# Optimization experiments

Hardware: AMD Instinct MI355X
Metric: run time of the kernel (lower is better)

Reference implementation:

```python
import jax, jax.numpy as jnp
from jax import lax
import numpy as np

EPS = 1e-5  # BatchNorm eps


def setup_inputs() -> dict:
    key = jax.random.key(0)
    ks = jax.random.split(key, 8)
    N, C_in, T, V = 64, 64, 300, 25
    C_out, K, KT = 64, 3, 9
    x = jax.random.normal(ks[0], (N, C_in, T, V), dtype=jnp.float32)
    A = jax.random.uniform(ks[1], (K, V, V), dtype=jnp.float32)
    # 1x1 conv weight squeezed to [K*C_out, C_in]
    w_gcn = jax.random.normal(ks[2], (K * C_out, C_in), dtype=jnp.float32) * (1.0 / np.sqrt(C_in))
    b_gcn = jax.random.normal(ks[3], (K * C_out,), dtype=jnp.float32) * 0.01
    # temporal conv weight [O, I, kT, 1]
    w_tcn = jax.random.normal(ks[4], (C_out, C_out, KT, 1), dtype=jnp.float32) * (1.0 / np.sqrt(C_out * KT))
    b_tcn = jax.random.normal(ks[5], (C_out,), dtype=jnp.float32) * 0.01
    gamma = jnp.ones((C_out,), dtype=jnp.float32)
    beta = jnp.zeros((C_out,), dtype=jnp.float32)
    return {"x": x, "A": A, "w_gcn": w_gcn, "b_gcn": b_gcn,
            "w_tcn": w_tcn, "b_tcn": b_tcn, "gamma": gamma, "beta": beta}


def reference(x, A, w_gcn, b_gcn, w_tcn, b_tcn, gamma, beta):
    K = A.shape[0]
    # unit_gcn: 1x1 conv (pointwise over channels) then spatial graph aggregation
    y = jnp.einsum('nctv,oc->notv', x, w_gcn) + b_gcn[None, :, None, None]  # [N, K*C, T, V]
    n, kc, t, v = y.shape
    y = y.reshape(n, K, kc // K, t, v)
    y = jnp.einsum('nkctv,kvw->nctw', y, A)  # [N, C, T, V]
    # unit_tcn: temporal conv (kernel 9x1, pad 4) + BatchNorm (training mode: batch stats)
    pad = (w_tcn.shape[2] - 1) // 2
    y = lax.conv_general_dilated(y, w_tcn, window_strides=(1, 1),
                                 padding=((pad, pad), (0, 0)),
                                 dimension_numbers=('NCHW', 'OIHW', 'NCHW'))
    y = y + b_tcn[None, :, None, None]
    mean = jnp.mean(y, axis=(0, 2, 3), keepdims=True)
    var = jnp.var(y, axis=(0, 2, 3), keepdims=True)
    y = (y - mean) * lax.rsqrt(var + EPS) * gamma[None, :, None, None] + beta[None, :, None, None]
    # residual (identity: in==out, stride==1) + ReLU
    return jax.nn.relu(y + x)
```

## Files before the change

### kernel.cpp

```cpp
#include <hip/hip_runtime.h>
#include <hip/hip_bf16.h>

#define N_    64
#define C_    64
#define T_    300
#define V_    25
#define K_    3
#define KT_   9
#define PAD_  4

typedef short bf16x8 __attribute__((ext_vector_type(8)));
typedef float f32x4  __attribute__((ext_vector_type(4)));

static __device__ __forceinline__ unsigned short f2bf(float f) {
    __hip_bfloat16 h = __float2bfloat16(f);
    return __builtin_bit_cast(unsigned short, h);
}
static __device__ __forceinline__ unsigned int pk2(float a, float b) {
    return (unsigned int)f2bf(a) | ((unsigned int)f2bf(b) << 16);
}
static __device__ __forceinline__ float bfhi(unsigned int u) {
    return __builtin_bit_cast(float, u << 16);
}
static __device__ __forceinline__ float bflo(unsigned int u) {
    return __builtin_bit_cast(float, u & 0xffff0000u);
}
static __device__ __forceinline__ float bf2f(unsigned short u) {
    return __builtin_bit_cast(float, (unsigned int)u << 16);
}

__global__ __launch_bounds__(256) void prep_kernel(
    const float* __restrict__ Wt, const float* __restrict__ Wg,
    const float* __restrict__ bg, const float* __restrict__ A,
    unsigned short* __restrict__ Wtb, unsigned short* __restrict__ Wgbt,
    unsigned short* __restrict__ bias2b, unsigned short* __restrict__ Abt)
{
    int i = blockIdx.x * 256 + threadIdx.x;
    if (i < 9*64*64) {
        int kt = i >> 12, r = i & 4095, o = r >> 6, c = r & 63;
        Wtb[i] = f2bf(Wt[(size_t)(o*64 + c)*9 + kt]);
    }
    int j = i - 9*64*64;
    if (j >= 0 && j < 64*192) {
        int o = j / 192, kc = j - 192*(j/192);
        int k = kc >> 6, ci = kc & 63;
        Wgbt[j] = f2bf(Wg[(size_t)(k*64 + o)*64 + ci]);
    }
    int m = j - 64*192;
    if (m >= 0 && m < 64*25) {
        int c = m / 25, w = m - 25*(m/25);
        float s = 0.f;
        for (int k = 0; k < 3; ++k) {
            float col = 0.f;
            for (int v = 0; v < 25; ++v) col += A[k*625 + v*25 + w];
            s += bg[k*64 + c] * col;
        }
        bias2b[w*64 + c] = f2bf(s);
    }
    int p = m - 64*25;
    if (p >= 0 && p < 3*32*40) {
        int k = p / 1280, r = p - 1280*k, w = r / 40, v = r - 40*(r/40);
        float val = (w < 25 && v < 25) ? A[k*625 + v*25 + w] : 0.f;
        Abt[p] = f2bf(val);
    }
}

#define GSUB   15
#define GGRP   (T_/GSUB)
#define NGBLK  (N_*GGRP)

__global__ __launch_bounds__(256, 5) void gcn_kernel(
    const float* __restrict__ x,
    const unsigned short* __restrict__ Wgbt,
    const unsigned short* __restrict__ Abt,
    const unsigned short* __restrict__ bias2b,
    unsigned short* __restrict__ y2)
{
    __shared__ unsigned short xslab[64*40];
    __shared__ unsigned short xa[32*200];
    __shared__ unsigned int   bias2L[25*34];

    const int tid  = threadIdx.x;
    const int n    = blockIdx.x / GGRP;
    const int tg   = (blockIdx.x % GGRP) * GSUB;
    const int lane = tid & 63, wave = tid >> 6;
    const int l15  = lane & 15, lq = lane >> 4;

    bf16x8 wfrag[6], afrag[6];
    #pragma unroll
    for (int cb = 0; cb < 6; ++cb) {
        wfrag[cb] = *(const bf16x8*)(Wgbt + (wave*16 + l15)*192 + cb*32 + lq*8);
        asm volatile("" : "+v"(wfrag[cb]));
    }
    #pragma unroll
    for (int s = 0; s < 6; ++s) {
        afrag[s] = *(const bf16x8*)(Abt + ((s >> 1)*32 + (s & 1)*16 + l15)*40 + lq*8);
        asm volatile("" : "+v"(afrag[s]));
    }

    for (int i = tid; i < 800; i += 256)
        bias2L[(i >> 5)*34 + (i & 31)] = ((const unsigned int*)bias2b)[i];
    if (tid < 192) {
        int r = tid / 3, z = tid - 3*(tid/3);
        ((unsigned int*)xslab)[r*20 + 13 + z] = 0u;
    }
    #pragma unroll
    for (int s = 0; s < 4; ++s) {
        int slot = tid + s*256;
        if (slot < 64*13) {
            int row = slot/13, sl = slot - 13*row;
            const float* xr = x + ((size_t)(n*C_ + row)*T_ + tg)*V_;
            float f0, f1;
            if (sl < 12) { float2 t2 = *(const float2*)(xr + 2*sl); f0 = t2.x; f1 = t2.y; }
            else         { f0 = xr[24]; f1 = 0.f; }
            ((unsigned int*)xslab)[row*20 + sl] = pk2(f0, f1);
        }
    }
    __syncthreads();

    for (int j = 0; j < GSUB; ++j) {
        const int t = tg + j;
        float2 Lr[4];
        const bool hn = (j + 1 < GSUB);
        if (hn) {
            #pragma unroll
            for (int s = 0; s < 4; ++s) {
                int slot = tid + s*256;
                if (slot < 64*13) {
                    int row = slot/13, sl = slot - 13*row;
                    const float* xr = x + ((size_t)(n*C_ + row)*T_ + t + 1)*V_;
                    if (sl < 12) Lr[s] = *(const float2*)(xr + 2*sl);
                    else         { Lr[s].x = xr[24]; Lr[s].y = 0.f; }
                }
            }
        }
        {
            bf16x8 xf = *(const bf16x8*)(xslab + (wave*16 + l15)*40 + lq*8);
            #pragma unroll
            for (int s = 0; s < 6; ++s) {
                f32x4 d = {};
                d = __builtin_amdgcn_mfma_f32_16x16x32_bf16(xf, afrag[s], d, 0, 0, 0);
                const int w = (s & 1)*16 + l15;
                if (w < 25) {
                    const int k = s >> 1;
                    unsigned long long pv = (unsigned long long)pk2(d[0], d[1])
                                          | ((unsigned long long)pk2(d[2], d[3]) << 32);
                    *(unsigned long long*)((char*)xa + w*400 + k*128 + wave*32 + lq*8) = pv;
                }
            }
        }
        __syncthreads();
        {
            f32x4 acc0 = {}, acc1 = {};
            #pragma unroll
            for (int cb = 0; cb < 6; ++cb) {
                bf16x8 b0 = *(const bf16x8*)((const char*)xa + l15*400      + cb*64 + lq*16);
                bf16x8 b1 = *(const bf16x8*)((const char*)xa + (16+l15)*400 + cb*64 + lq*16);
                acc0 = __builtin_amdgcn_mfma_f32_16x16x32_bf16(wfrag[cb], b0, acc0, 0, 0, 0);
                acc1 = __builtin_amdgcn_mfma_f32_16x16x32_bf16(wfrag[cb], b1, acc1, 0, 0, 0);
            }
            const int o0 = wave*16 + lq*4;
            {
                const int col = l15;
                unsigned int bu0 = bias2L[col*34 + (o0 >> 1)];
                unsigned int bu1 = bias2L[col*34 + (o0 >> 1) + 1];
                float v0 = acc0[0] + bfhi(bu0), v1 = acc0[1] + bflo(bu0);
                float v2 = acc0[2] + bfhi(bu1), v3 = acc0[3] + bflo(bu1);
                const size_t gcol = ((size_t)n*T_ + t)*V_ + col;
                *(unsigned long long*)(y2 + gcol*64 + o0) =
                      (unsigned long long)pk2(v0, v1)
                    | ((unsigned long long)pk2(v2, v3) << 32);
            }
            if (l15 < 9) {
                const int col = 16 + l15;
                unsigned int bu0 = bias2L[col*34 + (o0 >> 1)];
                unsigned int bu1 = bias2L[col*34 + (o0 >> 1) + 1];
                float v0 = acc1[0] + bfhi(bu0), v1 = acc1[1] + bflo(bu0);
                float v2 = acc1[2] + bfhi(bu1), v3 = acc1[3] + bflo(bu1);
                const size_t gcol = ((size_t)n*T_ + t)*V_ + col;
                *(unsigned long long*)(y2 + gcol*64 + o0) =
                      (unsigned long long)pk2(v0, v1)
                    | ((unsigned long long)pk2(v2, v3) << 32);
            }
        }
        if (hn) {
            #pragma unroll
            for (int s = 0; s < 4; ++s) {
                int slot = tid + s*256;
                if (slot < 64*13) {
                    int row = slot/13, sl = slot - 13*row;
                    ((unsigned int*)xslab)[row*20 + sl] = pk2(Lr[s].x, Lr[s].y);
                }
            }
        }
        __syncthreads();
    }
}

#define TTT    20
#define TCOLS  (TTT*V_)
#define SLABC  712
#define TTILES (T_/TTT)
#define NBLK   (N_*TTILES)

template<int BF>
__global__ __launch_bounds__(512, 2) void tcn_kernel(
    const unsigned short* __restrict__ y2, const unsigned short* __restrict__ Wtb,
    const float* __restrict__ bt,
    unsigned short* __restrict__ y3b, float* __restrict__ y3f,
    float* __restrict__ psum, float* __restrict__ psq)
{
    __shared__ unsigned short slab[SLABC*40];
    __shared__ float s_sum[64], s_sq[64];

    const int tid = threadIdx.x;
    const int n  = blockIdx.x / TTILES;
    const int t0 = (blockIdx.x % TTILES) * TTT;
    const int lane = tid & 63, wave = tid >> 6;
    const int l15 = lane & 15, lq = lane >> 4;
    const int colw = wave * 64;

    if (tid < 64) { s_sum[tid] = 0.f; s_sq[tid] = 0.f; }

    const int lo = (t0 < PAD_) ? (PAD_ - t0)*V_ : 0;
    const int hi = (t0 + TTT + PAD_ > T_) ? (T_ + PAD_ - t0)*V_ : SLABC;
    const long gbase = ((long)n*T_*V_ + (long)(t0 - PAD_)*V_)*64;

    f32x4 acc[4][4] = {};

    #pragma unroll
    for (int h = 0; h < 2; ++h) {
        __syncthreads();
        for (int i = tid; i < SLABC*4; i += 512) {
            int col = i >> 2, ck = i & 3;
            float4 val = {0.f, 0.f, 0.f, 0.f};
            if (col >= lo && col < hi)
                val = *(const float4*)(y2 + gbase + (long)col*64 + h*32 + ck*8);
            *(float4*)((char*)slab + col*80 + ck*16) = val;
        }
        __syncthreads();
        #pragma unroll
        for (int kt = 0; kt < 9; ++kt) {
            bf16x8 a[4];
            #pragma unroll
            for (int mt = 0; mt < 4; ++mt)
                a[mt] = *(const bf16x8*)(Wtb + kt*4096 + (mt*16 + l15)*64
                                         + h*32 + lq*8);
            #pragma unroll
            for (int nf = 0; nf < 4; ++nf) {
                const int col = colw + nf*16 + l15 + kt*25;
                bf16x8 b = *(const bf16x8*)((const char*)slab + col*80 + lq*16);
                #pragma unroll
                for (int mt = 0; mt < 4; ++mt)
                    acc[mt][nf] = __builtin_amdgcn_mfma_f32_16x16x32_bf16(
                        a[mt], b, acc[mt][nf], 0, 0, 0);
            }
        }
    }

    float ls[16], lsq[16];
    #pragma unroll
    for (int e = 0; e < 16; ++e) { ls[e] = 0.f; lsq[e] = 0.f; }

    #pragma unroll
    for (int mt = 0; mt < 4; ++mt) {
        #pragma unroll
        for (int r = 0; r < 4; ++r) {
            const int e = mt*4 + r;
            const int o = mt*16 + lq*4 + r;
            const float bias = bt[o];
            #pragma unroll
            for (int nf = 0; nf < 4; ++nf) {
                const int col = colw + nf*16 + l15;
                if (col < TCOLS) {
                    const float val = acc[mt][nf][r] + bias;
                    const size_t idx = (size_t)(n*C_ + o)*(T_*V_) + t0*V_ + col;
                    if (BF) y3b[idx] = f2bf(val);
                    else    y3f[idx] = val;
                    ls[e] += val; lsq[e] += val*val;
                }
            }
        }
    }

    __syncthreads();
    #pragma unroll
    for (int e = 0; e < 16; ++e) {
        float a = ls[e], b = lsq[e];
        a += __shfl_xor(a, 1); a += __shfl_xor(a, 2);
        a += __shfl_xor(a, 4); a += __shfl_xor(a, 8);
        b += __shfl_xor(b, 1); b += __shfl_xor(b, 2);
        b += __shfl_xor(b, 4); b += __shfl_xor(b, 8);
        if (l15 == 0) {
            const int o = (e >> 2)*16 + lq*4 + (e & 3);
            atomicAdd(&s_sum[o], a);
            atomicAdd(&s_sq[o], b);
        }
    }
    __syncthreads();
    if (tid < 64) {
        psum[(size_t)tid*NBLK + blockIdx.x] = s_sum[tid];
        psq [(size_t)tid*NBLK + blockIdx.x] = s_sq [tid];
    }
}

__global__ __launch_bounds__(256) void stats_kernel(
    const float* __restrict__ psum, const float* __restrict__ psq,
    const float* __restrict__ gamma, const float* __restrict__ beta,
    float* __restrict__ sb)
{
    const int o = blockIdx.x;
    const int tid = threadIdx.x;
    float s = 0.f, q = 0.f;
    for (int i = tid; i < NBLK; i += 256) {
        s += psum[(size_t)o*NBLK + i];
        q += psq [(size_t)o*NBLK + i];
    }
    __shared__ float rs[256], rq[256];
    rs[tid] = s; rq[tid] = q;
    __syncthreads();
    for (int off = 128; off > 0; off >>= 1) {
        if (tid < off) { rs[tid] += rs[tid + off]; rq[tid] += rq[tid + off]; }
        __syncthreads();
    }
    if (tid == 0) {
        const float cnt = (float)(N_ * T_ * V_);
        float mean = rs[0] / cnt;
        float var  = rq[0] / cnt - mean * mean;
        float rstd = rsqrtf(var + 1e-5f);
        float sc   = gamma[o] * rstd;
        sb[o]      = sc;
        sb[C_ + o] = beta[o] - mean * sc;
    }
}

__global__ __launch_bounds__(256) void bn_res_relu_bf16_kernel(
    const float* __restrict__ x, const unsigned short* __restrict__ y3b,
    const float* __restrict__ sb, float* __restrict__ out)
{
    const size_t total4 = (size_t)N_ * C_ * T_ * V_ / 4;
    size_t i4 = (size_t)blockIdx.x * 256 + threadIdx.x;
    if (i4 >= total4) return;
    const int c = (int)((i4 / (T_ * V_ / 4)) % C_);
    const float sc = sb[c], sh = sb[C_ + c];
    ushort4 yv = ((const ushort4*)y3b)[i4];
    float4 xv = ((const float4*)x)[i4];
    float4 o;
    o.x = fmaxf(bf2f(yv.x) * sc + sh + xv.x, 0.0f);
    o.y = fmaxf(bf2f(yv.y) * sc + sh + xv.y, 0.0f);
    o.z = fmaxf(bf2f(yv.z) * sc + sh + xv.z, 0.0f);
    o.w = fmaxf(bf2f(yv.w) * sc + sh + xv.w, 0.0f);
    ((float4*)out)[i4] = o;
}

__global__ __launch_bounds__(256) void bn_res_relu_f32_kernel(
    const float* __restrict__ x, const float* __restrict__ sb,
    float* __restrict__ y)
{
    const size_t total4 = (size_t)N_ * C_ * T_ * V_ / 4;
    size_t i4 = (size_t)blockIdx.x * 256 + threadIdx.x;
    if (i4 >= total4) return;
    const int c = (int)((i4 / (T_ * V_ / 4)) % C_);
    const float sc = sb[c], sh = sb[C_ + c];
    float4 yv = ((const float4*)y)[i4];
    float4 xv = ((const float4*)x)[i4];
    float4 o;
    o.x = fmaxf(yv.x * sc + sh + xv.x, 0.0f);
    o.y = fmaxf(yv.y * sc + sh + xv.y, 0.0f);
    o.z = fmaxf(yv.z * sc + sh + xv.z, 0.0f);
    o.w = fmaxf(yv.w * sc + sh + xv.w, 0.0f);
    ((float4*)y)[i4] = o;
}

extern "C" void kernel_launch(void* const* d_in, const int* in_sizes, int n_in,
                              void* d_out, int out_size, void* d_ws, size_t ws_size,
                              hipStream_t stream)
{
    const float* x     = (const float*)d_in[0];
    const float* A     = (const float*)d_in[1];
    const float* wg    = (const float*)d_in[2];
    const float* bg    = (const float*)d_in[3];
    const float* wt    = (const float*)d_in[4];
    const float* bt    = (const float*)d_in[5];
    const float* gamma = (const float*)d_in[6];
    const float* beta  = (const float*)d_in[7];
    float* out = (float*)d_out;

    char* wsb = (char*)d_ws;
    const size_t Y2B   = 61440000;
    const size_t Y3B   = 61440000;
    const size_t PSB   = (size_t)C_ * NBLK * 4;
    const size_t TABLE = 2*PSB + 512 + 73728 + 24576 + 3200 + 7680;
    const bool usebf = ws_size >= Y2B + Y3B + TABLE;

    unsigned short* y2  = (unsigned short*)wsb;
    unsigned short* y3b = (unsigned short*)(wsb + Y2B);
    const size_t base2  = usebf ? (Y2B + Y3B) : Y2B;
    float* psum            = (float*)(wsb + base2);
    float* psq             = (float*)(wsb + base2 + PSB);
    float* sb              = (float*)(wsb + base2 + 2*PSB);
    unsigned short* Wtb    = (unsigned short*)(wsb + base2 + 2*PSB + 512);
    unsigned short* Wgbt   = (unsigned short*)(wsb + base2 + 2*PSB + 512 + 73728);
    unsigned short* bias2b = (unsigned short*)(wsb + base2 + 2*PSB + 512 + 73728 + 24576);
    unsigned short* Abt    = (unsigned short*)(wsb + base2 + 2*PSB + 512 + 73728 + 24576 + 3200);

    prep_kernel<<<214, 256, 0, stream>>>(wt, wg, bg, A, Wtb, Wgbt, bias2b, Abt);
    gcn_kernel<<<NGBLK, 256, 0, stream>>>(x, Wgbt, Abt, bias2b, y2);
    if (usebf)
        tcn_kernel<1><<<NBLK, 512, 0, stream>>>(y2, Wtb, bt, y3b, out, psum, psq);
    else
        tcn_kernel<0><<<NBLK, 512, 0, stream>>>(y2, Wtb, bt, y3b, out, psum, psq);
    stats_kernel<<<C_, 256, 0, stream>>>(psum, psq, gamma, beta, sb);
    const size_t total4 = (size_t)N_ * C_ * T_ * V_ / 4;
    const int bnblk = (int)((total4 + 255) / 256);
    if (usebf)
        bn_res_relu_bf16_kernel<<<bnblk, 256, 0, stream>>>(x, y3b, sb, out);
    else
        bn_res_relu_f32_kernel<<<bnblk, 256, 0, stream>>>(x, sb, out);
}
```

Before: 290.6 us.

## Fuse graph conv and temporal conv into one kernel with an LDS slab

The separate gcn and tcn kernels are merged. Each 512-thread block now computes the graph-conv output for its 20 time steps plus a 4-step halo on each side, two steps per iteration. It writes the result into a 64-channel XOR-swizzled LDS slab, which the temporal conv then reads directly. This removes the global bf16 intermediate y2, a full write and read of roughly 61 MB, and one kernel launch. The price is recomputing the halo time steps in every block and a larger LDS footprint that likely limits blocks per CU. A block-index remap also spreads consecutive blocks across XCDs.

```diff
diff --git a/kernel.cpp b/kernel.cpp
--- a/kernel.cpp
+++ b/kernel.cpp
@@ -65,31 +65,43 @@
     }
 }
 
-#define GSUB   15
-#define GGRP   (T_/GSUB)
-#define NGBLK  (N_*GGRP)
-
-__global__ __launch_bounds__(256, 5) void gcn_kernel(
+#define FTT    20
+#define FSLABC 712
+#define FNBLK  (N_*(T_/FTT))
+
+template<int BF>
+__global__ __launch_bounds__(512, 2) void fused_kernel(
     const float* __restrict__ x,
     const unsigned short* __restrict__ Wgbt,
     const unsigned short* __restrict__ Abt,
     const unsigned short* __restrict__ bias2b,
-    unsigned short* __restrict__ y2)
-{
-    __shared__ unsigned short xslab[64*40];
-    __shared__ unsigned short xa[32*200];
+    const unsigned short* __restrict__ Wtb,
+    const float* __restrict__ bt,
+    unsigned short* __restrict__ y3b, float* __restrict__ y3f,
+    float* __restrict__ psum, float* __restrict__ psq)
+{
+    __shared__ unsigned short slab[FSLABC*64];
+    __shared__ unsigned short xa[64*200];
+    __shared__ unsigned short xslab[128*40];
     __shared__ unsigned int   bias2L[25*34];
+    __shared__ float s_sum[64], s_sq[64];
 
     const int tid  = threadIdx.x;
-    const int n    = blockIdx.x / GGRP;
-    const int tg   = (blockIdx.x % GGRP) * GSUB;
+    const int bid  = (int)((blockIdx.x & 7)*120 + (blockIdx.x >> 3));
+    const int n    = bid / (T_/FTT);
+    const int tg   = (bid % (T_/FTT)) * FTT;
     const int lane = tid & 63, wave = tid >> 6;
     const int l15  = lane & 15, lq = lane >> 4;
+    const int tp   = wave & 1, blk = wave >> 1;
+
+    const int t_begin = (tg >= PAD_) ? (tg - PAD_) : 0;
+    const int t_end   = (tg + FTT + PAD_ <= T_) ? (tg + FTT + PAD_) : T_;
+    const int P = (t_end - t_begin) >> 1;
 
     bf16x8 wfrag[6], afrag[6];
     #pragma unroll
     for (int cb = 0; cb < 6; ++cb) {
-        wfrag[cb] = *(const bf16x8*)(Wgbt + (wave*16 + l15)*192 + cb*32 + lq*8);
+        wfrag[cb] = *(const bf16x8*)(Wgbt + (blk*16 + l15)*192 + cb*32 + lq*8);
         asm volatile("" : "+v"(wfrag[cb]));
     }
     #pragma unroll
@@ -98,18 +110,21 @@
         asm volatile("" : "+v"(afrag[s]));
     }
 
-    for (int i = tid; i < 800; i += 256)
+    for (int i = tid; i < FSLABC*16; i += 512)
+        ((unsigned long long*)slab)[i] = 0ull;
+    for (int i = tid; i < 800; i += 512)
         bias2L[(i >> 5)*34 + (i & 31)] = ((const unsigned int*)bias2b)[i];
-    if (tid < 192) {
-        int r = tid / 3, z = tid - 3*(tid/3);
-        ((unsigned int*)xslab)[r*20 + 13 + z] = 0u;
+    if (tid < 128*3) {
+        int row = tid / 3, z = tid - 3*(tid/3);
+        ((unsigned int*)xslab)[row*20 + 13 + z] = 0u;
     }
     #pragma unroll
     for (int s = 0; s < 4; ++s) {
-        int slot = tid + s*256;
-        if (slot < 64*13) {
+        int slot = tid + s*512;
+        if (slot < 128*13) {
             int row = slot/13, sl = slot - 13*row;
-            const float* xr = x + ((size_t)(n*C_ + row)*T_ + tg)*V_;
+            int tpp = row >> 6, ci = row & 63;
+            const float* xr = x + ((size_t)(n*C_ + ci)*T_ + t_begin + tpp)*V_;
             float f0, f1;
             if (sl < 12) { float2 t2 = *(const float2*)(xr + 2*sl); f0 = t2.x; f1 = t2.y; }
             else         { f0 = xr[24]; f1 = 0.f; }
@@ -118,24 +133,25 @@
     }
     __syncthreads();
 
-    for (int j = 0; j < GSUB; ++j) {
-        const int t = tg + j;
+    for (int p = 0; p < P; ++p) {
+        const bool hn = (p + 1 < P);
         float2 Lr[4];
-        const bool hn = (j + 1 < GSUB);
         if (hn) {
             #pragma unroll
             for (int s = 0; s < 4; ++s) {
-                int slot = tid + s*256;
-                if (slot < 64*13) {
+                int slot = tid + s*512;
+                if (slot < 128*13) {
                     int row = slot/13, sl = slot - 13*row;
-                    const float* xr = x + ((size_t)(n*C_ + row)*T_ + t + 1)*V_;
+                    int tpp = row >> 6, ci = row & 63;
+                    const float* xr = x + ((size_t)(n*C_ + ci)*T_
+                                           + t_begin + 2*(p+1) + tpp)*V_;
                     if (sl < 12) Lr[s] = *(const float2*)(xr + 2*sl);
                     else         { Lr[s].x = xr[24]; Lr[s].y = 0.f; }
                 }
             }
         }
         {
-            bf16x8 xf = *(const bf16x8*)(xslab + (wave*16 + l15)*40 + lq*8);
+            bf16x8 xf = *(const bf16x8*)(xslab + (tp*64 + blk*16 + l15)*40 + lq*8);
             #pragma unroll
             for (int s = 0; s < 6; ++s) {
                 f32x4 d = {};
@@ -145,49 +161,54 @@
                     const int k = s >> 1;
                     unsigned long long pv = (unsigned long long)pk2(d[0], d[1])
                                           | ((unsigned long long)pk2(d[2], d[3]) << 32);
-                    *(unsigned long long*)((char*)xa + w*400 + k*128 + wave*32 + lq*8) = pv;
+                    *(unsigned long long*)((char*)xa + (tp*32 + w)*400
+                                           + k*128 + blk*32 + lq*8) = pv;
                 }
             }
         }
         __syncthreads();
         {
+            const int t = t_begin + 2*p + tp;
             f32x4 acc0 = {}, acc1 = {};
             #pragma unroll
             for (int cb = 0; cb < 6; ++cb) {
-                bf16x8 b0 = *(const bf16x8*)((const char*)xa + l15*400      + cb*64 + lq*16);
-                bf16x8 b1 = *(const bf16x8*)((const char*)xa + (16+l15)*400 + cb*64 + lq*16);
+                bf16x8 b0 = *(const bf16x8*)((const char*)xa
+                              + (tp*32 + l15)*400 + cb*64 + lq*16);
+                bf16x8 b1 = *(const bf16x8*)((const char*)xa
+                              + (tp*32 + 16 + l15)*400 + cb*64 + lq*16);
                 acc0 = __builtin_amdgcn_mfma_f32_16x16x32_bf16(wfrag[cb], b0, acc0, 0, 0, 0);
                 acc1 = __builtin_amdgcn_mfma_f32_16x16x32_bf16(wfrag[cb], b1, acc1, 0, 0, 0);
             }
-            const int o0 = wave*16 + lq*4;
+            const int lcb = (t - tg + PAD_)*25;
+            const int o0  = blk*16 + lq*4;
             {
-                const int col = l15;
-                unsigned int bu0 = bias2L[col*34 + (o0 >> 1)];
-                unsigned int bu1 = bias2L[col*34 + (o0 >> 1) + 1];
+                const int lc = lcb + l15;
+                unsigned int bu0 = bias2L[l15*34 + (o0 >> 1)];
+                unsigned int bu1 = bias2L[l15*34 + (o0 >> 1) + 1];
                 float v0 = acc0[0] + bfhi(bu0), v1 = acc0[1] + bflo(bu0);
                 float v2 = acc0[2] + bfhi(bu1), v3 = acc0[3] + bflo(bu1);
-                const size_t gcol = ((size_t)n*T_ + t)*V_ + col;
-                *(unsigned long long*)(y2 + gcol*64 + o0) =
-                      (unsigned long long)pk2(v0, v1)
-                    | ((unsigned long long)pk2(v2, v3) << 32);
+                unsigned long long pv = (unsigned long long)pk2(v0, v1)
+                                      | ((unsigned long long)pk2(v2, v3) << 32);
+                int byte = (lc*128 + o0*2) ^ ((lc & 7) << 4);
+                *(unsigned long long*)((char*)slab + byte) = pv;
             }
             if (l15 < 9) {
-                const int col = 16 + l15;
-                unsigned int bu0 = bias2L[col*34 + (o0 >> 1)];
-                unsigned int bu1 = bias2L[col*34 + (o0 >> 1) + 1];
+                const int lc = lcb + 16 + l15;
+                unsigned int bu0 = bias2L[(16 + l15)*34 + (o0 >> 1)];
+                unsigned int bu1 = bias2L[(16 + l15)*34 + (o0 >> 1) + 1];
                 float v0 = acc1[0] + bfhi(bu0), v1 = acc1[1] + bflo(bu0);
                 float v2 = acc1[2] + bfhi(bu1), v3 = acc1[3] + bflo(bu1);
-                const size_t gcol = ((size_t)n*T_ + t)*V_ + col;
-                *(unsigned long long*)(y2 + gcol*64 + o0) =
-                      (unsigned long long)pk2(v0, v1)
-                    | ((unsigned long long)pk2(v2, v3) << 32);
+                unsigned long long pv = (unsigned long long)pk2(v0, v1)
+                                      | ((unsigned long long)pk2(v2, v3) << 32);
+                int byte = (lc*128 + o0*2) ^ ((lc & 7) << 4);
+                *(unsigned long long*)((char*)slab + byte) = pv;
             }
         }
         if (hn) {
             #pragma unroll
             for (int s = 0; s < 4; ++s) {
-                int slot = tid + s*256;
-                if (slot < 64*13) {
+                int slot = tid + s*512;
+                if (slot < 128*13) {
                     int row = slot/13, sl = slot - 13*row;
                     ((unsigned int*)xslab)[row*20 + sl] = pk2(Lr[s].x, Lr[s].y);
                 }
@@ -195,61 +216,22 @@
         }
         __syncthreads();
     }
-}
-
-#define TTT    20
-#define TCOLS  (TTT*V_)
-#define SLABC  712
-#define TTILES (T_/TTT)
-#define NBLK   (N_*TTILES)
-
-template<int BF>
-__global__ __launch_bounds__(512, 2) void tcn_kernel(
-    const unsigned short* __restrict__ y2, const unsigned short* __restrict__ Wtb,
-    const float* __restrict__ bt,
-    unsigned short* __restrict__ y3b, float* __restrict__ y3f,
-    float* __restrict__ psum, float* __restrict__ psq)
-{
-    __shared__ unsigned short slab[SLABC*40];
-    __shared__ float s_sum[64], s_sq[64];
-
-    const int tid = threadIdx.x;
-    const int n  = blockIdx.x / TTILES;
-    const int t0 = (blockIdx.x % TTILES) * TTT;
-    const int lane = tid & 63, wave = tid >> 6;
-    const int l15 = lane & 15, lq = lane >> 4;
-    const int colw = wave * 64;
-
-    if (tid < 64) { s_sum[tid] = 0.f; s_sq[tid] = 0.f; }
-
-    const int lo = (t0 < PAD_) ? (PAD_ - t0)*V_ : 0;
-    const int hi = (t0 + TTT + PAD_ > T_) ? (T_ + PAD_ - t0)*V_ : SLABC;
-    const long gbase = ((long)n*T_*V_ + (long)(t0 - PAD_)*V_)*64;
 
     f32x4 acc[4][4] = {};
-
-    #pragma unroll
-    for (int h = 0; h < 2; ++h) {
-        __syncthreads();
-        for (int i = tid; i < SLABC*4; i += 512) {
-            int col = i >> 2, ck = i & 3;
-            float4 val = {0.f, 0.f, 0.f, 0.f};
-            if (col >= lo && col < hi)
-                val = *(const float4*)(y2 + gbase + (long)col*64 + h*32 + ck*8);
-            *(float4*)((char*)slab + col*80 + ck*16) = val;
-        }
-        __syncthreads();
+    #pragma unroll
+    for (int kt = 0; kt < 9; ++kt) {
         #pragma unroll
-        for (int kt = 0; kt < 9; ++kt) {
+        for (int cb = 0; cb < 2; ++cb) {
             bf16x8 a[4];
             #pragma unroll
             for (int mt = 0; mt < 4; ++mt)
                 a[mt] = *(const bf16x8*)(Wtb + kt*4096 + (mt*16 + l15)*64
-                                         + h*32 + lq*8);
+                                         + cb*32 + lq*8);
             #pragma unroll
             for (int nf = 0; nf < 4; ++nf) {
-                const int col = colw + nf*16 + l15 + kt*25;
-                bf16x8 b = *(const bf16x8*)((const char*)slab + col*80 + lq*16);
+                const int lc = wave*64 + nf*16 + l15 + kt*25;
+                int byte = (lc*128 + cb*64 + lq*16) ^ ((lc & 7) << 4);
+                bf16x8 b = *(const bf16x8*)((const char*)slab + byte);
                 #pragma unroll
                 for (int mt = 0; mt < 4; ++mt)
                     acc[mt][nf] = __builtin_amdgcn_mfma_f32_16x16x32_bf16(
@@ -261,7 +243,6 @@
     float ls[16], lsq[16];
     #pragma unroll
     for (int e = 0; e < 16; ++e) { ls[e] = 0.f; lsq[e] = 0.f; }
-
     #pragma unroll
     for (int mt = 0; mt < 4; ++mt) {
         #pragma unroll
@@ -271,10 +252,10 @@
             const float bias = bt[o];
             #pragma unroll
             for (int nf = 0; nf < 4; ++nf) {
-                const int col = colw + nf*16 + l15;
-                if (col < TCOLS) {
+                const int col = wave*64 + nf*16 + l15;
+                if (col < FTT*V_) {
                     const float val = acc[mt][nf][r] + bias;
-                    const size_t idx = (size_t)(n*C_ + o)*(T_*V_) + t0*V_ + col;
+                    const size_t idx = (size_t)(n*C_ + o)*(T_*V_) + tg*V_ + col;
                     if (BF) y3b[idx] = f2bf(val);
                     else    y3f[idx] = val;
                     ls[e] += val; lsq[e] += val*val;
@@ -283,6 +264,7 @@
         }
     }
 
+    if (tid < 64) { s_sum[tid] = 0.f; s_sq[tid] = 0.f; }
     __syncthreads();
     #pragma unroll
     for (int e = 0; e < 16; ++e) {
@@ -299,8 +281,8 @@
     }
     __syncthreads();
     if (tid < 64) {
-        psum[(size_t)tid*NBLK + blockIdx.x] = s_sum[tid];
-        psq [(size_t)tid*NBLK + blockIdx.x] = s_sq [tid];
+        psum[(size_t)tid*FNBLK + bid] = s_sum[tid];
+        psq [(size_t)tid*FNBLK + bid] = s_sq [tid];
     }
 }
 
@@ -312,9 +294,9 @@
     const int o = blockIdx.x;
     const int tid = threadIdx.x;
     float s = 0.f, q = 0.f;
-    for (int i = tid; i < NBLK; i += 256) {
-        s += psum[(size_t)o*NBLK + i];
-        q += psq [(size_t)o*NBLK + i];
+    for (int i = tid; i < FNBLK; i += 256) {
+        s += psum[(size_t)o*FNBLK + i];
+        q += psq [(size_t)o*FNBLK + i];
     }
     __shared__ float rs[256], rq[256];
     rs[tid] = s; rq[tid] = q;
@@ -387,15 +369,13 @@
     float* out = (float*)d_out;
 
     char* wsb = (char*)d_ws;
-    const size_t Y2B   = 61440000;
     const size_t Y3B   = 61440000;
-    const size_t PSB   = (size_t)C_ * NBLK * 4;
+    const size_t PSB   = (size_t)C_ * FNBLK * 4;
     const size_t TABLE = 2*PSB + 512 + 73728 + 24576 + 3200 + 7680;
-    const bool usebf = ws_size >= Y2B + Y3B + TABLE;
-
-    unsigned short* y2  = (unsigned short*)wsb;
-    unsigned short* y3b = (unsigned short*)(wsb + Y2B);
-    const size_t base2  = usebf ? (Y2B + Y3B) : Y2B;
+    const bool usebf = ws_size >= Y3B + TABLE;
+
+    unsigned short* y3b = (unsigned short*)wsb;
+    const size_t base2  = usebf ? Y3B : 0;
     float* psum            = (float*)(wsb + base2);
     float* psq             = (float*)(wsb + base2 + PSB);
     float* sb              = (float*)(wsb + base2 + 2*PSB);
@@ -405,11 +385,12 @@
     unsigned short* Abt    = (unsigned short*)(wsb + base2 + 2*PSB + 512 + 73728 + 24576 + 3200);
 
     prep_kernel<<<214, 256, 0, stream>>>(wt, wg, bg, A, Wtb, Wgbt, bias2b, Abt);
-    gcn_kernel<<<NGBLK, 256, 0, stream>>>(x, Wgbt, Abt, bias2b, y2);
     if (usebf)
-        tcn_kernel<1><<<NBLK, 512, 0, stream>>>(y2, Wtb, bt, y3b, out, psum, psq);
+        fused_kernel<1><<<FNBLK, 512, 0, stream>>>(x, Wgbt, Abt, bias2b, Wtb, bt,
+                                                   y3b, out, psum, psq);
     else
-        tcn_kernel<0><<<NBLK, 512, 0, stream>>>(y2, Wtb, bt, y3b, out, psum, psq);
+        fused_kernel<0><<<FNBLK, 512, 0, stream>>>(x, Wgbt, Abt, bias2b, Wtb, bt,
+                                                   y3b, out, psum, psq);
     stats_kernel<<<C_, 256, 0, stream>>>(psum, psq, gamma, beta, sb);
     const size_t total4 = (size_t)N_ * C_ * T_ * V_ / 4;
     const int bnblk = (int)((total4 + 255) / 256);
```

New measurement: 295.8 us. Within noise of the previous version (+1.8%).
